# Kernel optimization log

Measured on AMD Instinct MI355X. Metric: run time of the kernel, lower is better.

## Reference

```python
import jax, jax.numpy as jnp
import numpy as np

# Module config (mirrors TritonMoEConfig)
N_EMBD = 768
EXPERT_SIZES = [(8, 512), (8, 1024)]  # (count, width) pairs
TOP_K = 8
NORM_TOPK_PROB = True

EXPERT_WIDTHS = []
for cnt, w in EXPERT_SIZES:
    EXPERT_WIDTHS += [w] * cnt
EXPERT_OFFSETS = np.concatenate([[0], np.cumsum(EXPERT_WIDTHS)]).astype(np.int64)
NUM_EXPERTS = len(EXPERT_WIDTHS)          # 16
TOTAL_WIDTH = int(EXPERT_OFFSETS[-1])     # 12288


def setup_inputs() -> dict:
    key = jax.random.key(0)
    k1, k2, k3, k4 = jax.random.split(key, 4)
    x = jax.random.normal(k1, (1, 2048, N_EMBD), dtype=jnp.float32)
    # trunc_normal(std=0.02) approximated by clipped normal
    router_w = jax.random.normal(k2, (NUM_EXPERTS, N_EMBD), dtype=jnp.float32) * 0.02
    w1 = jnp.clip(jax.random.normal(k3, (N_EMBD, TOTAL_WIDTH), dtype=jnp.float32) * 0.02, -0.06, 0.06)
    w2 = jnp.clip(jax.random.normal(k4, (TOTAL_WIDTH, N_EMBD), dtype=jnp.float32) * 0.02, -0.06, 0.06)
    return {"x": x, "router_w": router_w, "w1": w1, "w2": w2}


def reference(x, router_w, w1, w2):
    B, S, D = x.shape
    xt = x.reshape(-1, D)                              # [T, D]
    T = xt.shape[0]
    # 1. Route tokens: softmax over experts, top-k selection
    logits = jnp.einsum('td,ed->te', xt, router_w)     # [T, E]
    probs = jax.nn.softmax(logits, axis=-1)
    topk_w, topk_idx = jax.lax.top_k(probs, TOP_K)     # [T, K]
    if NORM_TOPK_PROB:
        topk_w = topk_w / jnp.sum(topk_w, axis=-1, keepdims=True)
    # Per-token combine weight for every expert (0 if not selected): [T, E]
    comb = jnp.zeros((T, NUM_EXPERTS), dtype=xt.dtype)
    comb = comb.at[jnp.arange(T)[:, None], topk_idx].add(topk_w)
    # 2-6. Grouped GEMM up (with activation) + down, combine with routing weights.
    # Experts have distinct widths, so loop over the fixed expert list.
    out = jnp.zeros_like(xt)
    for e in range(NUM_EXPERTS):
        off = int(EXPERT_OFFSETS[e])
        wd = EXPERT_WIDTHS[e]
        h = jax.nn.gelu(xt @ w1[:, off:off + wd])      # [T, wd]
        out = out + comb[:, e:e + 1] * (h @ w2[off:off + wd, :])
    return out.reshape(B, S, D)
```

## Files before the change

### kernel.cpp

```cpp
#include <hip/hip_runtime.h>
#include <hip/hip_bf16.h>


#define T_TOK 2048
#define D_EMB 768
#define W_TOT 12288
#define N_EXP 16

typedef __attribute__((ext_vector_type(4))) float f32x4;
typedef __attribute__((ext_vector_type(8))) short bf16x8;

typedef __attribute__((address_space(1))) const unsigned int as1c_u32;
typedef __attribute__((address_space(3))) unsigned int as3_u32;

__device__ __forceinline__ void gload16(const void* g, void* l) {
  __builtin_amdgcn_global_load_lds((as1c_u32*)g, (as3_u32*)l, 16, 0, 0);
}

__device__ __forceinline__ unsigned short f2bf(float f) {
  __hip_bfloat16 h = __float2bfloat16(f);
  return *reinterpret_cast<unsigned short*>(&h);
}

__device__ __forceinline__ float gelu_f(float x) {
  float x3 = x * x * x;
  float a = 0.7978845608028654f * __builtin_fmaf(0.044715f, x3, x);
  a = fminf(fmaxf(a, -20.f), 20.f);
  float e = __expf(-2.0f * a);
  float t = (1.0f - e) / (1.0f + e);
  return 0.5f * x * (1.0f + t);
}

__global__ __launch_bounds__(256) void transpose_cvt_kernel(
    const float* __restrict__ in, unsigned short* __restrict__ out, int R, int C) {
  __shared__ float tile[32][33];
  int c0 = blockIdx.x * 32;
  int r0 = blockIdx.y * 32;
  int i = threadIdx.x;
  {
    int r = i >> 3, c4 = (i & 7) * 4;
    float4 v = *(const float4*)(in + (size_t)(r0 + r) * C + c0 + c4);
    tile[r][c4 + 0] = v.x; tile[r][c4 + 1] = v.y;
    tile[r][c4 + 2] = v.z; tile[r][c4 + 3] = v.w;
  }
  __syncthreads();
  {
    int c = i >> 3, r4 = (i & 7) * 4;
    ushort4 o;
    o.x = f2bf(tile[r4 + 0][c]);
    o.y = f2bf(tile[r4 + 1][c]);
    o.z = f2bf(tile[r4 + 2][c]);
    o.w = f2bf(tile[r4 + 3][c]);
    *(ushort4*)(out + (size_t)(c0 + c) * R + r0 + r4) = o;
  }
}


__global__ __launch_bounds__(256) void router_kernel(
    const float* __restrict__ x, const float* __restrict__ rw,
    float* __restrict__ comb, unsigned short* __restrict__ xbout) {
  int tid = threadIdx.x, lane = tid & 63, w = tid >> 6;
  int t = blockIdx.x * 4 + w;
  const float* xr = x + (size_t)t * D_EMB;
  float xv[12];
#pragma unroll
  for (int i = 0; i < 12; ++i) xv[i] = xr[lane + 64 * i];
#pragma unroll
  for (int i = 0; i < 12; ++i)
    xbout[(size_t)t * D_EMB + lane + 64 * i] = f2bf(xv[i]);
  float lg[16];
#pragma unroll
  for (int e = 0; e < 16; ++e) {
    const float* we = rw + (size_t)e * D_EMB;
    float p = 0.f;
#pragma unroll
    for (int i = 0; i < 12; ++i) p = __builtin_fmaf(xv[i], we[lane + 64 * i], p);
#pragma unroll
    for (int off = 32; off >= 1; off >>= 1) p += __shfl_xor(p, off, 64);
    lg[e] = p;
  }
  float mx = lg[0];
#pragma unroll
  for (int e = 1; e < 16; ++e) mx = fmaxf(mx, lg[e]);
  float ex[16];
#pragma unroll
  for (int e = 0; e < 16; ++e) ex[e] = __expf(lg[e] - mx);
  float selsum = 0.f, myval = 0.f;
#pragma unroll
  for (int e = 0; e < 16; ++e) {
    int rank = 0;
#pragma unroll
    for (int e2 = 0; e2 < 16; ++e2)
      rank += (ex[e2] > ex[e]) || (ex[e2] == ex[e] && e2 < e);
    bool sel = rank < 8;
    float v = sel ? ex[e] : 0.f;
    selsum += v;
    if (e == lane) myval = v;
  }
  if (lane < 16) comb[(size_t)t * N_EXP + lane] = myval / selsum;
}


template <int EPI, int MAP>
__global__ __launch_bounds__(512, 2) void gemm_kernel(
    const unsigned short* __restrict__ Ag, const unsigned short* __restrict__ Bg,
    int lda, int ldb, int ntiles, int kchunk,
    const float* __restrict__ comb, unsigned short* __restrict__ hout,
    float* __restrict__ pout) {
  __shared__ __align__(16) char smem[114688];

  const int tid = threadIdx.x;
  const int lane = tid & 63;
  const int wid = tid >> 6;
  const int wr = wid >> 2;
  const int wc = wid & 3;

  int mt, nt, zt;
  {
    int bid = blockIdx.x;
    if (MAP == 0) {
      int xcd = bid & 7, r = bid >> 3;
      nt = xcd * 8 + (r >> 3); mt = r & 7; zt = 0;
    } else {
      zt = bid & 7; int r = bid >> 3;
      nt = r & 3; mt = r >> 2;
    }
  }
  const int rm0 = mt * 256;
  const int cn0 = nt * 192;
  const int kbeg = zt * kchunk;

  auto gsrc = [&](const unsigned short* base, int ld, int row0, int j) {
    int off = j * 8192 + tid * 16;
    int row = off >> 7, inrow = off & 127;
    int scol = inrow ^ ((row & 7) << 4);
    return (const char*)base + ((size_t)(row0 + row) * ld + kbeg) * 2 + scol;
  };
  const char* pA0 = gsrc(Ag, lda, rm0, 0);
  const char* pA1 = gsrc(Ag, lda, rm0, 1);
  const char* pA2 = gsrc(Ag, lda, rm0, 2);
  const char* pA3 = gsrc(Ag, lda, rm0, 3);
  const char* pB0 = gsrc(Bg, ldb, cn0, 0);
  const char* pB1 = gsrc(Bg, ldb, cn0, 1);
  const char* pB2 = gsrc(Bg, ldb, cn0, 2);

  const int lswz = (lane & 7) << 4;
  const int colk0 = (((lane >> 4) & 3) * 16) ^ lswz;
  const int colk1 = (64 + ((lane >> 4) & 3) * 16) ^ lswz;
  const int abase0 = wr * 16384 + (lane & 15) * 128 + colk0;
  const int abase1 = wr * 16384 + (lane & 15) * 128 + colk1;
  const int bb0 = wc * 6144 + (lane & 15) * 128 + colk0;
  const int bb1 = wc * 6144 + (lane & 15) * 128 + colk1;

  f32x4 acc[8][3];
#pragma unroll
  for (int m = 0; m < 8; ++m)
#pragma unroll
    for (int n = 0; n < 3; ++n) acc[m][n] = (f32x4){0.f, 0.f, 0.f, 0.f};

  gload16(pB0, smem + 65536 + wid * 1024);
  gload16(pB1, smem + 65536 + 8192 + wid * 1024);
  gload16(pB2, smem + 65536 + 16384 + wid * 1024);
  gload16(pA0, smem + wid * 1024);
  gload16(pA2, smem + 16384 + wid * 1024);
  gload16(pA1, smem + 8192 + wid * 1024);
  gload16(pA3, smem + 24576 + wid * 1024);
  pA0 += 128; pA1 += 128; pA2 += 128; pA3 += 128;
  pB0 += 128; pB1 += 128; pB2 += 128;
  __builtin_amdgcn_sched_barrier(0);

  int aoff = 0, boff = 0;
  bf16x8 af[4], ag[4], bfr[3], bgr[3];
  for (int t = 0; t < ntiles; ++t) {
    const int adst = aoff ^ 32768;
    const int bdst = boff ^ 24576;

    asm volatile("s_waitcnt vmcnt(2)" ::: "memory");
    __builtin_amdgcn_s_barrier();
    __builtin_amdgcn_sched_barrier(0);
#pragma unroll
    for (int m = 0; m < 4; ++m) {
      af[m] = *(const bf16x8*)(smem + aoff + abase0 + m * 2048);
      ag[m] = *(const bf16x8*)(smem + aoff + abase1 + m * 2048);
    }
#pragma unroll
    for (int n = 0; n < 3; ++n) {
      bfr[n] = *(const bf16x8*)(smem + 65536 + boff + bb0 + n * 2048);
      bgr[n] = *(const bf16x8*)(smem + 65536 + boff + bb1 + n * 2048);
    }
    gload16(pB0, smem + 65536 + bdst + wid * 1024);
    gload16(pB1, smem + 65536 + bdst + 8192 + wid * 1024);
    gload16(pB2, smem + 65536 + bdst + 16384 + wid * 1024);
    gload16(pA0, smem + adst + wid * 1024);
    gload16(pA2, smem + adst + 16384 + wid * 1024);
    __builtin_amdgcn_sched_barrier(0);
    __builtin_amdgcn_s_setprio(1);
#pragma unroll
    for (int m = 0; m < 4; ++m)
#pragma unroll
      for (int n = 0; n < 3; ++n) {
        acc[m][n] = __builtin_amdgcn_mfma_f32_16x16x32_bf16(af[m], bfr[n], acc[m][n], 0, 0, 0);
        acc[m][n] = __builtin_amdgcn_mfma_f32_16x16x32_bf16(ag[m], bgr[n], acc[m][n], 0, 0, 0);
      }
    __builtin_amdgcn_s_setprio(0);

    asm volatile("s_waitcnt vmcnt(5)" ::: "memory");
    __builtin_amdgcn_s_barrier();
    __builtin_amdgcn_sched_barrier(0);
#pragma unroll
    for (int m = 0; m < 4; ++m) {
      af[m] = *(const bf16x8*)(smem + aoff + abase0 + 8192 + m * 2048);
      ag[m] = *(const bf16x8*)(smem + aoff + abase1 + 8192 + m * 2048);
    }
    gload16(pA1, smem + adst + 8192 + wid * 1024);
    gload16(pA3, smem + adst + 24576 + wid * 1024);
    __builtin_amdgcn_sched_barrier(0);
    __builtin_amdgcn_s_setprio(1);
#pragma unroll
    for (int m = 0; m < 4; ++m)
#pragma unroll
      for (int n = 0; n < 3; ++n) {
        acc[4 + m][n] = __builtin_amdgcn_mfma_f32_16x16x32_bf16(af[m], bfr[n], acc[4 + m][n], 0, 0, 0);
        acc[4 + m][n] = __builtin_amdgcn_mfma_f32_16x16x32_bf16(ag[m], bgr[n], acc[4 + m][n], 0, 0, 0);
      }
    __builtin_amdgcn_s_setprio(0);

    pA0 += 128; pA1 += 128; pA2 += 128; pA3 += 128;
    pB0 += 128; pB1 += 128; pB2 += 128;
    aoff = adst; boff = bdst;
  }

  asm volatile("s_waitcnt vmcnt(0)" ::: "memory");
  __syncthreads();

  const int r0 = (lane >> 4) * 4;
  const int cl = lane & 15;
  if constexpr (EPI == 1) {
    float* Cwf = (float*)smem;
    {
      int row = tid >> 1, c8 = (tid & 1) * 8;
      const float* s = comb + (size_t)(rm0 + row) * N_EXP + c8;
      *(float4*)&Cwf[row * 16 + c8] = *(const float4*)s;
      *(float4*)&Cwf[row * 16 + c8 + 4] = *(const float4*)(s + 4);
    }
    __syncthreads();
#pragma unroll
    for (int n = 0; n < 3; ++n) {
      int colg = cn0 + wc * 48 + n * 16 + cl;
      int e = (colg < 4096) ? (colg >> 9) : (8 + ((colg - 4096) >> 10));
#pragma unroll
      for (int m = 0; m < 8; ++m) {
        int rl = wr * 128 + m * 16 + r0;
#pragma unroll
        for (int r = 0; r < 4; ++r) {
          float v = gelu_f(acc[m][n][r]) * Cwf[(rl + r) * 16 + e];
          hout[(size_t)(rm0 + rl + r) * W_TOT + colg] = f2bf(v);
        }
      }
    }
  } else {
    float* pz = pout + (size_t)zt * T_TOK * D_EMB;
#pragma unroll
    for (int n = 0; n < 3; ++n) {
      int colg = cn0 + wc * 48 + n * 16 + cl;
#pragma unroll
      for (int m = 0; m < 8; ++m) {
        int rl = wr * 128 + m * 16 + r0;
#pragma unroll
        for (int r = 0; r < 4; ++r)
          pz[(size_t)(rm0 + rl + r) * D_EMB + colg] = acc[m][n][r];
      }
    }
  }
}

__global__ __launch_bounds__(256) void reduce_kernel(
    const float* __restrict__ partial, float* __restrict__ out, int splits) {
  int i = (blockIdx.x * 256 + threadIdx.x) * 4;
  if (i >= T_TOK * D_EMB) return;
  float4 s = *(const float4*)(partial + i);
  for (int sp = 1; sp < splits; ++sp) {
    float4 v = *(const float4*)(partial + (size_t)sp * T_TOK * D_EMB + i);
    s.x += v.x; s.y += v.y; s.z += v.z; s.w += v.w;
  }
  *(float4*)(out + i) = s;
}


extern "C" void kernel_launch(void* const* d_in, const int* in_sizes, int n_in,
                              void* d_out, int out_size, void* d_ws, size_t ws_size,
                              hipStream_t stream) {
  const float* x = (const float*)d_in[0];
  const float* router_w = (const float*)d_in[1];
  const float* w1 = (const float*)d_in[2];
  const float* w2 = (const float*)d_in[3];
  float* out = (float*)d_out;

  char* ws = (char*)d_ws;
  size_t off = 0;
  auto alloc = [&](size_t bytes) {
    char* p = ws + off;
    off += (bytes + 255) & ~(size_t)255;
    return p;
  };
  unsigned short* xb  = (unsigned short*)alloc((size_t)T_TOK * D_EMB * 2);
  unsigned short* w1t = (unsigned short*)alloc((size_t)W_TOT * D_EMB * 2);
  unsigned short* w2t = (unsigned short*)alloc((size_t)D_EMB * W_TOT * 2);
  unsigned short* h   = (unsigned short*)alloc((size_t)T_TOK * W_TOT * 2);
  float* comb         = (float*)alloc((size_t)T_TOK * N_EXP * 4);

  const int splits = 8;
  float* partial = (float*)alloc((size_t)splits * T_TOK * D_EMB * 4);
  int kchunk = W_TOT / splits;

  transpose_cvt_kernel<<<dim3(W_TOT / 32, D_EMB / 32), 256, 0, stream>>>(w1, w1t, D_EMB, W_TOT);
  transpose_cvt_kernel<<<dim3(D_EMB / 32, W_TOT / 32), 256, 0, stream>>>(w2, w2t, W_TOT, D_EMB);
  router_kernel<<<T_TOK / 4, 256, 0, stream>>>(x, router_w, comb, xb);

  gemm_kernel<1, 0><<<512, 512, 0, stream>>>(
      xb, w1t, D_EMB, D_EMB, D_EMB / 64, D_EMB, comb, h, nullptr);

  gemm_kernel<0, 1><<<256, 512, 0, stream>>>(
      h, w2t, W_TOT, W_TOT, kchunk / 64, kchunk, nullptr, nullptr, partial);

  reduce_kernel<<<(T_TOK * D_EMB) / 1024, 256, 0, stream>>>(partial, out, splits);
}
```

Before: 136.9 us.

## Enlarge GEMM tile to 256x256 with four-phase quadrant-staged LDS pipeline

Widens the GEMM output tile from 256x192 to 256x256, so each wave holds an 8x4 accumulator block and the grids shrink to 384 and 192 blocks. The main loop is restructured into four sub-phases that each compute one quadrant of the accumulators while staging the next A and B halves into LDS. LDS grows to 128 KB and sync points are re-placed with extra barriers and lgkmcnt waits. The goal is higher arithmetic intensity and fewer blocks. The costs are more barriers, less occupancy (the 128 KB LDS likely allows one block per CU despite launch_bounds 2), and a grid smaller than two waves.

```diff
diff --git a/kernel.cpp b/kernel.cpp
--- a/kernel.cpp
+++ b/kernel.cpp
@@ -107,7 +107,7 @@
     int lda, int ldb, int ntiles, int kchunk,
     const float* __restrict__ comb, unsigned short* __restrict__ hout,
     float* __restrict__ pout) {
-  __shared__ __align__(16) char smem[114688];
+  __shared__ __align__(16) char smem[131072];
 
   const int tid = threadIdx.x;
   const int lane = tid & 63;
@@ -120,114 +120,171 @@
     int bid = blockIdx.x;
     if (MAP == 0) {
       int xcd = bid & 7, r = bid >> 3;
-      nt = xcd * 8 + (r >> 3); mt = r & 7; zt = 0;
+      nt = xcd * 6 + (r >> 3); mt = r & 7; zt = 0;
     } else {
       zt = bid & 7; int r = bid >> 3;
-      nt = r & 3; mt = r >> 2;
+      nt = r % 3; mt = r / 3;
     }
   }
   const int rm0 = mt * 256;
-  const int cn0 = nt * 192;
+  const int cn0 = nt * 256;
   const int kbeg = zt * kchunk;
 
-  auto gsrc = [&](const unsigned short* base, int ld, int row0, int j) {
+  auto gsrcA = [&](int h, int j) {
     int off = j * 8192 + tid * 16;
     int row = off >> 7, inrow = off & 127;
     int scol = inrow ^ ((row & 7) << 4);
-    return (const char*)base + ((size_t)(row0 + row) * ld + kbeg) * 2 + scol;
+    return (const char*)Ag +
+           ((size_t)(rm0 + h * 128 + row) * lda + kbeg) * 2 + scol;
   };
-  const char* pA0 = gsrc(Ag, lda, rm0, 0);
-  const char* pA1 = gsrc(Ag, lda, rm0, 1);
-  const char* pA2 = gsrc(Ag, lda, rm0, 2);
-  const char* pA3 = gsrc(Ag, lda, rm0, 3);
-  const char* pB0 = gsrc(Bg, ldb, cn0, 0);
-  const char* pB1 = gsrc(Bg, ldb, cn0, 1);
-  const char* pB2 = gsrc(Bg, ldb, cn0, 2);
+  auto gsrcB = [&](int h, int j) {
+    int off = j * 8192 + tid * 16;
+    int row = off >> 7, inrow = off & 127;
+    int scol = inrow ^ ((row & 7) << 4);
+    return (const char*)Bg +
+           ((size_t)(cn0 + h * 128 + row) * ldb + kbeg) * 2 + scol;
+  };
+  const char* qA00 = gsrcA(0, 0); const char* qA01 = gsrcA(0, 1);
+  const char* qA10 = gsrcA(1, 0); const char* qA11 = gsrcA(1, 1);
+  const char* qB00 = gsrcB(0, 0); const char* qB01 = gsrcB(0, 1);
+  const char* qB10 = gsrcB(1, 0); const char* qB11 = gsrcB(1, 1);
 
   const int lswz = (lane & 7) << 4;
   const int colk0 = (((lane >> 4) & 3) * 16) ^ lswz;
   const int colk1 = (64 + ((lane >> 4) & 3) * 16) ^ lswz;
-  const int abase0 = wr * 16384 + (lane & 15) * 128 + colk0;
-  const int abase1 = wr * 16384 + (lane & 15) * 128 + colk1;
-  const int bb0 = wc * 6144 + (lane & 15) * 128 + colk0;
-  const int bb1 = wc * 6144 + (lane & 15) * 128 + colk1;
-
-  f32x4 acc[8][3];
+  const int ab0 = wr * 16384 + (lane & 15) * 128 + colk0;
+  const int ab1 = wr * 16384 + (lane & 15) * 128 + colk1;
+  const int bb0 = 65536 + (wc >> 1) * 16384 + ((wc & 1) * 64 + (lane & 15)) * 128 + colk0;
+  const int bb1 = 65536 + (wc >> 1) * 16384 + ((wc & 1) * 64 + (lane & 15)) * 128 + colk1;
+
+  f32x4 acc[8][4];
 #pragma unroll
   for (int m = 0; m < 8; ++m)
 #pragma unroll
-    for (int n = 0; n < 3; ++n) acc[m][n] = (f32x4){0.f, 0.f, 0.f, 0.f};
-
-  gload16(pB0, smem + 65536 + wid * 1024);
-  gload16(pB1, smem + 65536 + 8192 + wid * 1024);
-  gload16(pB2, smem + 65536 + 16384 + wid * 1024);
-  gload16(pA0, smem + wid * 1024);
-  gload16(pA2, smem + 16384 + wid * 1024);
-  gload16(pA1, smem + 8192 + wid * 1024);
-  gload16(pA3, smem + 24576 + wid * 1024);
-  pA0 += 128; pA1 += 128; pA2 += 128; pA3 += 128;
-  pB0 += 128; pB1 += 128; pB2 += 128;
+    for (int n = 0; n < 4; ++n) acc[m][n] = (f32x4){0.f, 0.f, 0.f, 0.f};
+
+  gload16(qA00, smem + 0 + wid * 1024);
+  gload16(qA01, smem + 8192 + wid * 1024);
+  gload16(qA10, smem + 16384 + wid * 1024);
+  gload16(qA11, smem + 16384 + 8192 + wid * 1024);
+  gload16(qB00, smem + 65536 + wid * 1024);
+  gload16(qB01, smem + 65536 + 8192 + wid * 1024);
+  gload16(qB10, smem + 65536 + 16384 + wid * 1024);
+  gload16(qB11, smem + 65536 + 16384 + 8192 + wid * 1024);
+  gload16(qB00 + 128, smem + 65536 + 32768 + wid * 1024);
+  gload16(qB01 + 128, smem + 65536 + 32768 + 8192 + wid * 1024);
+  gload16(qB10 + 128, smem + 65536 + 32768 + 16384 + wid * 1024);
+  gload16(qB11 + 128, smem + 65536 + 32768 + 16384 + 8192 + wid * 1024);
+  const char* pA00 = qA00 + 128; const char* pA01 = qA01 + 128;
+  const char* pA10 = qA10 + 128; const char* pA11 = qA11 + 128;
+  const char* pB00 = qB00 + 256; const char* pB01 = qB01 + 256;
+  const char* pB10 = qB10 + 256; const char* pB11 = qB11 + 256;
+  asm volatile("s_waitcnt vmcnt(4)" ::: "memory");
+  __builtin_amdgcn_s_barrier();
   __builtin_amdgcn_sched_barrier(0);
 
-  int aoff = 0, boff = 0;
-  bf16x8 af[4], ag[4], bfr[3], bgr[3];
+  bf16x8 a[4][2], b0[2][2], b1[2][2];
+  int cb = 0;
   for (int t = 0; t < ntiles; ++t) {
-    const int adst = aoff ^ 32768;
-    const int bdst = boff ^ 24576;
-
-    asm volatile("s_waitcnt vmcnt(2)" ::: "memory");
-    __builtin_amdgcn_s_barrier();
-    __builtin_amdgcn_sched_barrier(0);
+    const int nb = cb ^ 32768;
+
 #pragma unroll
     for (int m = 0; m < 4; ++m) {
-      af[m] = *(const bf16x8*)(smem + aoff + abase0 + m * 2048);
-      ag[m] = *(const bf16x8*)(smem + aoff + abase1 + m * 2048);
-    }
-#pragma unroll
-    for (int n = 0; n < 3; ++n) {
-      bfr[n] = *(const bf16x8*)(smem + 65536 + boff + bb0 + n * 2048);
-      bgr[n] = *(const bf16x8*)(smem + 65536 + boff + bb1 + n * 2048);
-    }
-    gload16(pB0, smem + 65536 + bdst + wid * 1024);
-    gload16(pB1, smem + 65536 + bdst + 8192 + wid * 1024);
-    gload16(pB2, smem + 65536 + bdst + 16384 + wid * 1024);
-    gload16(pA0, smem + adst + wid * 1024);
-    gload16(pA2, smem + adst + 16384 + wid * 1024);
+      a[m][0] = *(const bf16x8*)(smem + cb + ab0 + m * 2048);
+      a[m][1] = *(const bf16x8*)(smem + cb + ab1 + m * 2048);
+    }
+#pragma unroll
+    for (int n = 0; n < 2; ++n) {
+      b0[n][0] = *(const bf16x8*)(smem + cb + bb0 + n * 2048);
+      b0[n][1] = *(const bf16x8*)(smem + cb + bb1 + n * 2048);
+    }
+    gload16(pA00, smem + nb + wid * 1024);
+    gload16(pA01, smem + nb + 8192 + wid * 1024);
+    pA00 += 128; pA01 += 128;
+    __builtin_amdgcn_s_barrier();
+    asm volatile("s_waitcnt lgkmcnt(0)" ::: "memory");
     __builtin_amdgcn_sched_barrier(0);
     __builtin_amdgcn_s_setprio(1);
 #pragma unroll
     for (int m = 0; m < 4; ++m)
 #pragma unroll
-      for (int n = 0; n < 3; ++n) {
-        acc[m][n] = __builtin_amdgcn_mfma_f32_16x16x32_bf16(af[m], bfr[n], acc[m][n], 0, 0, 0);
-        acc[m][n] = __builtin_amdgcn_mfma_f32_16x16x32_bf16(ag[m], bgr[n], acc[m][n], 0, 0, 0);
-      }
+      for (int n = 0; n < 2; ++n)
+#pragma unroll
+        for (int kk = 0; kk < 2; ++kk)
+          acc[m][n] = __builtin_amdgcn_mfma_f32_16x16x32_bf16(
+              a[m][kk], b0[n][kk], acc[m][n], 0, 0, 0);
     __builtin_amdgcn_s_setprio(0);
-
-    asm volatile("s_waitcnt vmcnt(5)" ::: "memory");
-    __builtin_amdgcn_s_barrier();
-    __builtin_amdgcn_sched_barrier(0);
+    __builtin_amdgcn_s_barrier();
+    __builtin_amdgcn_sched_barrier(0);
+
+#pragma unroll
+    for (int n = 0; n < 2; ++n) {
+      b1[n][0] = *(const bf16x8*)(smem + cb + bb0 + 4096 + n * 2048);
+      b1[n][1] = *(const bf16x8*)(smem + cb + bb1 + 4096 + n * 2048);
+    }
+    gload16(pA10, smem + nb + 16384 + wid * 1024);
+    gload16(pA11, smem + nb + 16384 + 8192 + wid * 1024);
+    pA10 += 128; pA11 += 128;
+    __builtin_amdgcn_s_barrier();
+    asm volatile("s_waitcnt lgkmcnt(0)" ::: "memory");
+    __builtin_amdgcn_sched_barrier(0);
+    __builtin_amdgcn_s_setprio(1);
+#pragma unroll
+    for (int m = 0; m < 4; ++m)
+#pragma unroll
+      for (int n = 0; n < 2; ++n)
+#pragma unroll
+        for (int kk = 0; kk < 2; ++kk)
+          acc[m][2 + n] = __builtin_amdgcn_mfma_f32_16x16x32_bf16(
+              a[m][kk], b1[n][kk], acc[m][2 + n], 0, 0, 0);
+    __builtin_amdgcn_s_setprio(0);
+    __builtin_amdgcn_s_barrier();
+    __builtin_amdgcn_sched_barrier(0);
+
 #pragma unroll
     for (int m = 0; m < 4; ++m) {
-      af[m] = *(const bf16x8*)(smem + aoff + abase0 + 8192 + m * 2048);
-      ag[m] = *(const bf16x8*)(smem + aoff + abase1 + 8192 + m * 2048);
-    }
-    gload16(pA1, smem + adst + 8192 + wid * 1024);
-    gload16(pA3, smem + adst + 24576 + wid * 1024);
+      a[m][0] = *(const bf16x8*)(smem + cb + ab0 + 8192 + m * 2048);
+      a[m][1] = *(const bf16x8*)(smem + cb + ab1 + 8192 + m * 2048);
+    }
+    gload16(pB00, smem + 65536 + cb + wid * 1024);
+    gload16(pB01, smem + 65536 + cb + 8192 + wid * 1024);
+    pB00 += 128; pB01 += 128;
+    __builtin_amdgcn_s_barrier();
+    asm volatile("s_waitcnt lgkmcnt(0)" ::: "memory");
     __builtin_amdgcn_sched_barrier(0);
     __builtin_amdgcn_s_setprio(1);
 #pragma unroll
     for (int m = 0; m < 4; ++m)
 #pragma unroll
-      for (int n = 0; n < 3; ++n) {
-        acc[4 + m][n] = __builtin_amdgcn_mfma_f32_16x16x32_bf16(af[m], bfr[n], acc[4 + m][n], 0, 0, 0);
-        acc[4 + m][n] = __builtin_amdgcn_mfma_f32_16x16x32_bf16(ag[m], bgr[n], acc[4 + m][n], 0, 0, 0);
-      }
+      for (int n = 0; n < 2; ++n)
+#pragma unroll
+        for (int kk = 0; kk < 2; ++kk)
+          acc[4 + m][2 + n] = __builtin_amdgcn_mfma_f32_16x16x32_bf16(
+              a[m][kk], b1[n][kk], acc[4 + m][2 + n], 0, 0, 0);
     __builtin_amdgcn_s_setprio(0);
-
-    pA0 += 128; pA1 += 128; pA2 += 128; pA3 += 128;
-    pB0 += 128; pB1 += 128; pB2 += 128;
-    aoff = adst; boff = bdst;
+    __builtin_amdgcn_s_barrier();
+    __builtin_amdgcn_sched_barrier(0);
+
+    gload16(pB10, smem + 65536 + cb + 16384 + wid * 1024);
+    gload16(pB11, smem + 65536 + cb + 16384 + 8192 + wid * 1024);
+    pB10 += 128; pB11 += 128;
+    asm volatile("s_waitcnt vmcnt(4)" ::: "memory");
+    __builtin_amdgcn_s_barrier();
+    __builtin_amdgcn_sched_barrier(0);
+    __builtin_amdgcn_s_setprio(1);
+#pragma unroll
+    for (int m = 0; m < 4; ++m)
+#pragma unroll
+      for (int n = 0; n < 2; ++n)
+#pragma unroll
+        for (int kk = 0; kk < 2; ++kk)
+          acc[4 + m][n] = __builtin_amdgcn_mfma_f32_16x16x32_bf16(
+              a[m][kk], b0[n][kk], acc[4 + m][n], 0, 0, 0);
+    __builtin_amdgcn_s_setprio(0);
+    __builtin_amdgcn_s_barrier();
+    __builtin_amdgcn_sched_barrier(0);
+
+    cb = nb;
   }
 
   asm volatile("s_waitcnt vmcnt(0)" ::: "memory");
@@ -245,8 +302,8 @@
     }
     __syncthreads();
 #pragma unroll
-    for (int n = 0; n < 3; ++n) {
-      int colg = cn0 + wc * 48 + n * 16 + cl;
+    for (int n = 0; n < 4; ++n) {
+      int colg = cn0 + wc * 64 + n * 16 + cl;
       int e = (colg < 4096) ? (colg >> 9) : (8 + ((colg - 4096) >> 10));
 #pragma unroll
       for (int m = 0; m < 8; ++m) {
@@ -261,8 +318,8 @@
   } else {
     float* pz = pout + (size_t)zt * T_TOK * D_EMB;
 #pragma unroll
-    for (int n = 0; n < 3; ++n) {
-      int colg = cn0 + wc * 48 + n * 16 + cl;
+    for (int n = 0; n < 4; ++n) {
+      int colg = cn0 + wc * 64 + n * 16 + cl;
 #pragma unroll
       for (int m = 0; m < 8; ++m) {
         int rl = wr * 128 + m * 16 + r0;
@@ -317,10 +374,10 @@
   transpose_cvt_kernel<<<dim3(D_EMB / 32, W_TOT / 32), 256, 0, stream>>>(w2, w2t, W_TOT, D_EMB);
   router_kernel<<<T_TOK / 4, 256, 0, stream>>>(x, router_w, comb, xb);
 
-  gemm_kernel<1, 0><<<512, 512, 0, stream>>>(
+  gemm_kernel<1, 0><<<384, 512, 0, stream>>>(
       xb, w1t, D_EMB, D_EMB, D_EMB / 64, D_EMB, comb, h, nullptr);
 
-  gemm_kernel<0, 1><<<256, 512, 0, stream>>>(
+  gemm_kernel<0, 1><<<192, 512, 0, stream>>>(
       h, w2t, W_TOT, W_TOT, kchunk / 64, kchunk, nullptr, nullptr, partial);
 
   reduce_kernel<<<(T_TOK * D_EMB) / 1024, 256, 0, stream>>>(partial, out, splits);
```

Result: slower. 158.9 us (+16.0%).

## Shrink GEMM tiles to 256x128 with K=32 steps for higher occupancy

Applied to the files above, without the earlier changes.

Reworks both grouped GEMMs to use 256x128 output tiles with a 32-wide K step, so the kernel needs 48 KB of LDS instead of 112 KB and launch bounds allow 4 blocks per CU. It also changes the swizzle and load mapping, makes the leading dimension a template constant, and raises the down-projection split-K from 8 to 16 when workspace allows. The aim is more resident waves and more blocks to hide latency and fill the CUs. The trade-off is less data reuse per tile, twice the barriers per K, and a larger partial buffer for the reduce kernel to sum.

```diff
diff --git a/kernel.cpp b/kernel.cpp
--- a/kernel.cpp
+++ b/kernel.cpp
@@ -101,13 +101,13 @@
 }
 
 
-template <int EPI, int MAP>
-__global__ __launch_bounds__(512, 2) void gemm_kernel(
+template <int EPI, int MAP, int LD>
+__global__ __launch_bounds__(512, 4) void gemm_kernel(
     const unsigned short* __restrict__ Ag, const unsigned short* __restrict__ Bg,
-    int lda, int ldb, int ntiles, int kchunk,
+    int ntiles, int kchunk, int splits,
     const float* __restrict__ comb, unsigned short* __restrict__ hout,
     float* __restrict__ pout) {
-  __shared__ __align__(16) char smem[114688];
+  __shared__ __align__(16) char smem[49152];
 
   const int tid = threadIdx.x;
   const int lane = tid & 63;
@@ -120,114 +120,82 @@
     int bid = blockIdx.x;
     if (MAP == 0) {
       int xcd = bid & 7, r = bid >> 3;
-      nt = xcd * 8 + (r >> 3); mt = r & 7; zt = 0;
+      nt = xcd * 12 + (r >> 3); mt = r & 7; zt = 0;
     } else {
-      zt = bid & 7; int r = bid >> 3;
-      nt = r & 3; mt = r >> 2;
+      zt = bid % splits; int rr = bid / splits;
+      nt = rr % 6; mt = rr / 6;
     }
   }
   const int rm0 = mt * 256;
-  const int cn0 = nt * 192;
+  const int cn0 = nt * 128;
   const int kbeg = zt * kchunk;
 
-  auto gsrc = [&](const unsigned short* base, int ld, int row0, int j) {
-    int off = j * 8192 + tid * 16;
-    int row = off >> 7, inrow = off & 127;
-    int scol = inrow ^ ((row & 7) << 4);
-    return (const char*)base + ((size_t)(row0 + row) * ld + kbeg) * 2 + scol;
-  };
-  const char* pA0 = gsrc(Ag, lda, rm0, 0);
-  const char* pA1 = gsrc(Ag, lda, rm0, 1);
-  const char* pA2 = gsrc(Ag, lda, rm0, 2);
-  const char* pA3 = gsrc(Ag, lda, rm0, 3);
-  const char* pB0 = gsrc(Bg, ldb, cn0, 0);
-  const char* pB1 = gsrc(Bg, ldb, cn0, 1);
-  const char* pB2 = gsrc(Bg, ldb, cn0, 2);
-
-  const int lswz = (lane & 7) << 4;
-  const int colk0 = (((lane >> 4) & 3) * 16) ^ lswz;
-  const int colk1 = (64 + ((lane >> 4) & 3) * 16) ^ lswz;
-  const int abase0 = wr * 16384 + (lane & 15) * 128 + colk0;
-  const int abase1 = wr * 16384 + (lane & 15) * 128 + colk1;
-  const int bb0 = wc * 6144 + (lane & 15) * 128 + colk0;
-  const int bb1 = wc * 6144 + (lane & 15) * 128 + colk1;
-
-  f32x4 acc[8][3];
+  const int s = tid >> 2;
+  const int scol = ((tid & 3) ^ (s & 3)) << 4;
+  const int rA = (s & 63) + ((s >> 6) << 7);
+  const char* pA0 = (const char*)Ag + ((size_t)(rm0 + rA) * LD + kbeg) * 2 + scol;
+  const char* pA1 = pA0 + (size_t)64 * LD * 2;
+  const char* pB  = (const char*)Bg + ((size_t)(cn0 + s) * LD + kbeg) * 2 + scol;
+
+  const int slot = ((lane >> 4) ^ (lane & 3)) << 4;
+  const int abase = wr * 4096 + (lane & 15) * 64 + slot;
+  const int bbase = 32768 + (wc * 32 + (lane & 15)) * 64 + slot;
+
+  f32x4 acc[8][2];
 #pragma unroll
   for (int m = 0; m < 8; ++m)
 #pragma unroll
-    for (int n = 0; n < 3; ++n) acc[m][n] = (f32x4){0.f, 0.f, 0.f, 0.f};
-
-  gload16(pB0, smem + 65536 + wid * 1024);
-  gload16(pB1, smem + 65536 + 8192 + wid * 1024);
-  gload16(pB2, smem + 65536 + 16384 + wid * 1024);
+    for (int n = 0; n < 2; ++n) acc[m][n] = (f32x4){0.f, 0.f, 0.f, 0.f};
+
+  gload16(pB, smem + 32768 + wid * 1024);
   gload16(pA0, smem + wid * 1024);
-  gload16(pA2, smem + 16384 + wid * 1024);
   gload16(pA1, smem + 8192 + wid * 1024);
-  gload16(pA3, smem + 24576 + wid * 1024);
-  pA0 += 128; pA1 += 128; pA2 += 128; pA3 += 128;
-  pB0 += 128; pB1 += 128; pB2 += 128;
+  pB += 64; pA0 += 64; pA1 += 64;
   __builtin_amdgcn_sched_barrier(0);
 
   int aoff = 0, boff = 0;
-  bf16x8 af[4], ag[4], bfr[3], bgr[3];
+  bf16x8 a[4], b[2];
   for (int t = 0; t < ntiles; ++t) {
-    const int adst = aoff ^ 32768;
-    const int bdst = boff ^ 24576;
+    const int nA = aoff ^ 16384;
+    const int nB = boff ^ 8192;
+
+    asm volatile("s_waitcnt vmcnt(1)" ::: "memory");
+    __builtin_amdgcn_s_barrier();
+    __builtin_amdgcn_sched_barrier(0);
+#pragma unroll
+    for (int m = 0; m < 4; ++m)
+      a[m] = *(const bf16x8*)(smem + aoff + abase + m * 1024);
+    b[0] = *(const bf16x8*)(smem + boff + bbase);
+    b[1] = *(const bf16x8*)(smem + boff + bbase + 1024);
+    gload16(pB, smem + 32768 + nB + wid * 1024);
+    gload16(pA0, smem + nA + wid * 1024);
+    __builtin_amdgcn_sched_barrier(0);
+    __builtin_amdgcn_s_setprio(1);
+#pragma unroll
+    for (int m = 0; m < 4; ++m) {
+      acc[m][0] = __builtin_amdgcn_mfma_f32_16x16x32_bf16(a[m], b[0], acc[m][0], 0, 0, 0);
+      acc[m][1] = __builtin_amdgcn_mfma_f32_16x16x32_bf16(a[m], b[1], acc[m][1], 0, 0, 0);
+    }
+    __builtin_amdgcn_s_setprio(0);
 
     asm volatile("s_waitcnt vmcnt(2)" ::: "memory");
     __builtin_amdgcn_s_barrier();
     __builtin_amdgcn_sched_barrier(0);
 #pragma unroll
+    for (int m = 0; m < 4; ++m)
+      a[m] = *(const bf16x8*)(smem + aoff + 8192 + abase + m * 1024);
+    gload16(pA1, smem + nA + 8192 + wid * 1024);
+    pB += 64; pA0 += 64; pA1 += 64;
+    __builtin_amdgcn_sched_barrier(0);
+    __builtin_amdgcn_s_setprio(1);
+#pragma unroll
     for (int m = 0; m < 4; ++m) {
-      af[m] = *(const bf16x8*)(smem + aoff + abase0 + m * 2048);
-      ag[m] = *(const bf16x8*)(smem + aoff + abase1 + m * 2048);
-    }
-#pragma unroll
-    for (int n = 0; n < 3; ++n) {
-      bfr[n] = *(const bf16x8*)(smem + 65536 + boff + bb0 + n * 2048);
-      bgr[n] = *(const bf16x8*)(smem + 65536 + boff + bb1 + n * 2048);
-    }
-    gload16(pB0, smem + 65536 + bdst + wid * 1024);
-    gload16(pB1, smem + 65536 + bdst + 8192 + wid * 1024);
-    gload16(pB2, smem + 65536 + bdst + 16384 + wid * 1024);
-    gload16(pA0, smem + adst + wid * 1024);
-    gload16(pA2, smem + adst + 16384 + wid * 1024);
-    __builtin_amdgcn_sched_barrier(0);
-    __builtin_amdgcn_s_setprio(1);
-#pragma unroll
-    for (int m = 0; m < 4; ++m)
-#pragma unroll
-      for (int n = 0; n < 3; ++n) {
-        acc[m][n] = __builtin_amdgcn_mfma_f32_16x16x32_bf16(af[m], bfr[n], acc[m][n], 0, 0, 0);
-        acc[m][n] = __builtin_amdgcn_mfma_f32_16x16x32_bf16(ag[m], bgr[n], acc[m][n], 0, 0, 0);
-      }
+      acc[4 + m][0] = __builtin_amdgcn_mfma_f32_16x16x32_bf16(a[m], b[0], acc[4 + m][0], 0, 0, 0);
+      acc[4 + m][1] = __builtin_amdgcn_mfma_f32_16x16x32_bf16(a[m], b[1], acc[4 + m][1], 0, 0, 0);
+    }
     __builtin_amdgcn_s_setprio(0);
 
-    asm volatile("s_waitcnt vmcnt(5)" ::: "memory");
-    __builtin_amdgcn_s_barrier();
-    __builtin_amdgcn_sched_barrier(0);
-#pragma unroll
-    for (int m = 0; m < 4; ++m) {
-      af[m] = *(const bf16x8*)(smem + aoff + abase0 + 8192 + m * 2048);
-      ag[m] = *(const bf16x8*)(smem + aoff + abase1 + 8192 + m * 2048);
-    }
-    gload16(pA1, smem + adst + 8192 + wid * 1024);
-    gload16(pA3, smem + adst + 24576 + wid * 1024);
-    __builtin_amdgcn_sched_barrier(0);
-    __builtin_amdgcn_s_setprio(1);
-#pragma unroll
-    for (int m = 0; m < 4; ++m)
-#pragma unroll
-      for (int n = 0; n < 3; ++n) {
-        acc[4 + m][n] = __builtin_amdgcn_mfma_f32_16x16x32_bf16(af[m], bfr[n], acc[4 + m][n], 0, 0, 0);
-        acc[4 + m][n] = __builtin_amdgcn_mfma_f32_16x16x32_bf16(ag[m], bgr[n], acc[4 + m][n], 0, 0, 0);
-      }
-    __builtin_amdgcn_s_setprio(0);
-
-    pA0 += 128; pA1 += 128; pA2 += 128; pA3 += 128;
-    pB0 += 128; pB1 += 128; pB2 += 128;
-    aoff = adst; boff = bdst;
+    aoff = nA; boff = nB;
   }
 
   asm volatile("s_waitcnt vmcnt(0)" ::: "memory");
@@ -239,14 +207,14 @@
     float* Cwf = (float*)smem;
     {
       int row = tid >> 1, c8 = (tid & 1) * 8;
-      const float* s = comb + (size_t)(rm0 + row) * N_EXP + c8;
-      *(float4*)&Cwf[row * 16 + c8] = *(const float4*)s;
-      *(float4*)&Cwf[row * 16 + c8 + 4] = *(const float4*)(s + 4);
+      const float* sc = comb + (size_t)(rm0 + row) * N_EXP + c8;
+      *(float4*)&Cwf[row * 16 + c8] = *(const float4*)sc;
+      *(float4*)&Cwf[row * 16 + c8 + 4] = *(const float4*)(sc + 4);
     }
     __syncthreads();
 #pragma unroll
-    for (int n = 0; n < 3; ++n) {
-      int colg = cn0 + wc * 48 + n * 16 + cl;
+    for (int n = 0; n < 2; ++n) {
+      int colg = cn0 + wc * 32 + n * 16 + cl;
       int e = (colg < 4096) ? (colg >> 9) : (8 + ((colg - 4096) >> 10));
 #pragma unroll
       for (int m = 0; m < 8; ++m) {
@@ -261,8 +229,8 @@
   } else {
     float* pz = pout + (size_t)zt * T_TOK * D_EMB;
 #pragma unroll
-    for (int n = 0; n < 3; ++n) {
-      int colg = cn0 + wc * 48 + n * 16 + cl;
+    for (int n = 0; n < 2; ++n) {
+      int colg = cn0 + wc * 32 + n * 16 + cl;
 #pragma unroll
       for (int m = 0; m < 8; ++m) {
         int rl = wr * 128 + m * 16 + r0;
@@ -278,12 +246,12 @@
     const float* __restrict__ partial, float* __restrict__ out, int splits) {
   int i = (blockIdx.x * 256 + threadIdx.x) * 4;
   if (i >= T_TOK * D_EMB) return;
-  float4 s = *(const float4*)(partial + i);
+  float4 sv = *(const float4*)(partial + i);
   for (int sp = 1; sp < splits; ++sp) {
     float4 v = *(const float4*)(partial + (size_t)sp * T_TOK * D_EMB + i);
-    s.x += v.x; s.y += v.y; s.z += v.z; s.w += v.w;
-  }
-  *(float4*)(out + i) = s;
+    sv.x += v.x; sv.y += v.y; sv.z += v.z; sv.w += v.w;
+  }
+  *(float4*)(out + i) = sv;
 }
 
 
@@ -309,7 +277,9 @@
   unsigned short* h   = (unsigned short*)alloc((size_t)T_TOK * W_TOT * 2);
   float* comb         = (float*)alloc((size_t)T_TOK * N_EXP * 4);
 
-  const int splits = 8;
+  int splits = 16;
+  if (off + (size_t)16 * T_TOK * D_EMB * 4 > ws_size) splits = 8;
+  if (off + (size_t)8 * T_TOK * D_EMB * 4 > ws_size) splits = 4;
   float* partial = (float*)alloc((size_t)splits * T_TOK * D_EMB * 4);
   int kchunk = W_TOT / splits;
 
@@ -317,11 +287,11 @@
   transpose_cvt_kernel<<<dim3(D_EMB / 32, W_TOT / 32), 256, 0, stream>>>(w2, w2t, W_TOT, D_EMB);
   router_kernel<<<T_TOK / 4, 256, 0, stream>>>(x, router_w, comb, xb);
 
-  gemm_kernel<1, 0><<<512, 512, 0, stream>>>(
-      xb, w1t, D_EMB, D_EMB, D_EMB / 64, D_EMB, comb, h, nullptr);
-
-  gemm_kernel<0, 1><<<256, 512, 0, stream>>>(
-      h, w2t, W_TOT, W_TOT, kchunk / 64, kchunk, nullptr, nullptr, partial);
+  gemm_kernel<1, 0, D_EMB><<<768, 512, 0, stream>>>(
+      xb, w1t, D_EMB / 32, D_EMB, 1, comb, h, nullptr);
+
+  gemm_kernel<0, 1, W_TOT><<<48 * splits, 512, 0, stream>>>(
+      h, w2t, kchunk / 32, kchunk, splits, nullptr, nullptr, partial);
 
   reduce_kernel<<<(T_TOK * D_EMB) / 1024, 256, 0, stream>>>(partial, out, splits);
 }
```

Result: slower. 163.1 us (+19.1%).

## Replace dense GEMMs with token-gathered grouped MoE GEMMs over routed tokens

Applied to the files above, without the earlier changes.

The router now builds per-expert token lists with atomics, storing token, top-k slot and combine weight, in place of a dense combine matrix. Both GEMMs become grouped per-expert GEMMs. The up-projection gathers routed token rows and writes a compact per-expert h buffer, and the down-projection scatters rows into per-slot partial buffers, which an 8-way reduction then sums. Because each token picks 8 of 16 experts, this skips about half of the dense FLOPs. In exchange it adds gather/scatter indirection, padding to 256-row tiles, nondeterministic token ordering from the atomics, and a larger 256x256 tile with 128KB of shared memory.

```diff
diff --git a/kernel.cpp b/kernel.cpp
--- a/kernel.cpp
+++ b/kernel.cpp
@@ -58,7 +58,8 @@
 
 __global__ __launch_bounds__(256) void router_kernel(
     const float* __restrict__ x, const float* __restrict__ rw,
-    float* __restrict__ comb, unsigned short* __restrict__ xbout) {
+    unsigned short* __restrict__ xbout, int* __restrict__ toklist,
+    float* __restrict__ combw, int* __restrict__ cnt) {
   int tid = threadIdx.x, lane = tid & 63, w = tid >> 6;
   int t = blockIdx.x * 4 + w;
   const float* xr = x + (size_t)t * D_EMB;
@@ -86,6 +87,7 @@
 #pragma unroll
   for (int e = 0; e < 16; ++e) ex[e] = __expf(lg[e] - mx);
   float selsum = 0.f, myval = 0.f;
+  bool mysel = false;
 #pragma unroll
   for (int e = 0; e < 16; ++e) {
     int rank = 0;
@@ -95,19 +97,26 @@
     bool sel = rank < 8;
     float v = sel ? ex[e] : 0.f;
     selsum += v;
-    if (e == lane) myval = v;
-  }
-  if (lane < 16) comb[(size_t)t * N_EXP + lane] = myval / selsum;
-}
-
-
-template <int EPI, int MAP>
-__global__ __launch_bounds__(512, 2) void gemm_kernel(
-    const unsigned short* __restrict__ Ag, const unsigned short* __restrict__ Bg,
-    int lda, int ldb, int ntiles, int kchunk,
-    const float* __restrict__ comb, unsigned short* __restrict__ hout,
-    float* __restrict__ pout) {
-  __shared__ __align__(16) char smem[114688];
+    if (e == lane) { myval = v; mysel = sel; }
+  }
+  unsigned long long mask = __ballot(lane < 16 && mysel);
+  if (lane < 16 && mysel) {
+    int slot = __popcll(mask & ((1ull << lane) - 1));
+    int pos = atomicAdd(&cnt[lane], 1);
+    toklist[lane * 2048 + pos] = t | (slot << 16);
+    combw[lane * 2048 + pos] = myval / selsum;
+  }
+}
+
+
+template <int MODE>
+__global__ __launch_bounds__(512, 2) void moe_gemm_kernel(
+    const unsigned short* __restrict__ Abase,
+    const unsigned short* __restrict__ Bbase,
+    const int* __restrict__ toklist, const float* __restrict__ combw,
+    const int* __restrict__ cnt, unsigned short* __restrict__ hbuf,
+    float* __restrict__ partial, float* __restrict__ dump) {
+  __shared__ __align__(16) char smem[131072];
 
   const int tid = threadIdx.x;
   const int lane = tid & 63;
@@ -115,171 +124,193 @@
   const int wr = wid >> 2;
   const int wc = wid & 3;
 
-  int mt, nt, zt;
+  int e, W, offe, mt, nt;
+  int hb;
   {
     int bid = blockIdx.x;
-    if (MAP == 0) {
-      int xcd = bid & 7, r = bid >> 3;
-      nt = xcd * 8 + (r >> 3); mt = r & 7; zt = 0;
+    if (MODE == 0) {
+      if (bid < 128) {
+        e = bid >> 4; int r = bid & 15; mt = r >> 1; nt = r & 1;
+        W = 512; offe = e * 512; hb = e * (2048 * 512);
+      } else {
+        int b = bid - 128; int el = b >> 5; int r = b & 31; mt = r >> 2; nt = r & 3;
+        e = el + 8; W = 1024; offe = 4096 + el * 1024;
+        hb = 8 * (2048 * 512) + el * (2048 * 1024);
+      }
     } else {
-      zt = bid & 7; int r = bid >> 3;
-      nt = r & 3; mt = r >> 2;
-    }
-  }
+      int bb = bid;
+      if (bid < 192) {
+        int el = bb / 24; e = el; W = 512; offe = el * 512; hb = el * (2048 * 512);
+        bb -= el * 24;
+      } else {
+        bb -= 192; int el = bb / 24; e = el + 8; W = 1024;
+        offe = 4096 + el * 1024; hb = 8 * (2048 * 512) + el * (2048 * 1024);
+        bb -= el * 24;
+      }
+      mt = bb / 3; nt = bb - mt * 3;
+    }
+  }
+  const int ce = cnt[e];
+  const int cpad = (ce + 255) & ~255;
   const int rm0 = mt * 256;
-  const int cn0 = nt * 192;
-  const int kbeg = zt * kchunk;
-
-  auto gsrc = [&](const unsigned short* base, int ld, int row0, int j) {
-    int off = j * 8192 + tid * 16;
-    int row = off >> 7, inrow = off & 127;
-    int scol = inrow ^ ((row & 7) << 4);
-    return (const char*)base + ((size_t)(row0 + row) * ld + kbeg) * 2 + scol;
-  };
-  const char* pA0 = gsrc(Ag, lda, rm0, 0);
-  const char* pA1 = gsrc(Ag, lda, rm0, 1);
-  const char* pA2 = gsrc(Ag, lda, rm0, 2);
-  const char* pA3 = gsrc(Ag, lda, rm0, 3);
-  const char* pB0 = gsrc(Bg, ldb, cn0, 0);
-  const char* pB1 = gsrc(Bg, ldb, cn0, 1);
-  const char* pB2 = gsrc(Bg, ldb, cn0, 2);
+  if (rm0 >= cpad) return;
+  const int cn0 = nt * 256;
+  const int ntiles = (MODE == 0) ? (D_EMB / 64) : (W >> 6);
+
+  const int srow = tid >> 3;
+  const int scol = ((tid & 7) * 16) ^ ((srow & 7) << 4);
+  const char* pA[4];
+#pragma unroll
+  for (int j = 0; j < 4; ++j) {
+    int i = rm0 + j * 64 + srow;
+    size_t rowoff;
+    if (MODE == 0) {
+      int tok = (i < ce) ? (toklist[e * 2048 + i] & 0xFFFF) : 0;
+      rowoff = (size_t)tok * D_EMB;
+    } else {
+      rowoff = (size_t)hb + (size_t)i * W;
+    }
+    pA[j] = (const char*)Abase + rowoff * 2 + scol;
+  }
+  const char* pB[4];
+#pragma unroll
+  for (int j = 0; j < 4; ++j) {
+    int r = cn0 + j * 64 + srow;
+    size_t rowoff = (MODE == 0) ? ((size_t)(offe + r) * D_EMB)
+                                : ((size_t)r * W_TOT + offe);
+    pB[j] = (const char*)Bbase + rowoff * 2 + scol;
+  }
 
   const int lswz = (lane & 7) << 4;
   const int colk0 = (((lane >> 4) & 3) * 16) ^ lswz;
   const int colk1 = (64 + ((lane >> 4) & 3) * 16) ^ lswz;
-  const int abase0 = wr * 16384 + (lane & 15) * 128 + colk0;
-  const int abase1 = wr * 16384 + (lane & 15) * 128 + colk1;
-  const int bb0 = wc * 6144 + (lane & 15) * 128 + colk0;
-  const int bb1 = wc * 6144 + (lane & 15) * 128 + colk1;
-
-  f32x4 acc[8][3];
+  const int ab0 = wr * 16384 + (lane & 15) * 128 + colk0;
+  const int ab1 = wr * 16384 + (lane & 15) * 128 + colk1;
+  const int bb0 = wc * 8192 + (lane & 15) * 128 + colk0;
+  const int bb1 = wc * 8192 + (lane & 15) * 128 + colk1;
+
+  f32x4 acc[8][4];
 #pragma unroll
   for (int m = 0; m < 8; ++m)
 #pragma unroll
-    for (int n = 0; n < 3; ++n) acc[m][n] = (f32x4){0.f, 0.f, 0.f, 0.f};
-
-  gload16(pB0, smem + 65536 + wid * 1024);
-  gload16(pB1, smem + 65536 + 8192 + wid * 1024);
-  gload16(pB2, smem + 65536 + 16384 + wid * 1024);
-  gload16(pA0, smem + wid * 1024);
-  gload16(pA2, smem + 16384 + wid * 1024);
-  gload16(pA1, smem + 8192 + wid * 1024);
-  gload16(pA3, smem + 24576 + wid * 1024);
-  pA0 += 128; pA1 += 128; pA2 += 128; pA3 += 128;
-  pB0 += 128; pB1 += 128; pB2 += 128;
+    for (int n = 0; n < 4; ++n) acc[m][n] = (f32x4){0.f, 0.f, 0.f, 0.f};
+
+#pragma unroll
+  for (int j = 0; j < 4; ++j) gload16(pB[j], smem + 65536 + j * 8192 + wid * 1024);
+  gload16(pA[0], smem + wid * 1024);
+  gload16(pA[2], smem + 16384 + wid * 1024);
+  gload16(pA[1], smem + 8192 + wid * 1024);
+  gload16(pA[3], smem + 24576 + wid * 1024);
+#pragma unroll
+  for (int j = 0; j < 4; ++j) { pA[j] += 128; pB[j] += 128; }
   __builtin_amdgcn_sched_barrier(0);
 
-  int aoff = 0, boff = 0;
-  bf16x8 af[4], ag[4], bfr[3], bgr[3];
+  int aoff = 0, boff = 65536;
+  bf16x8 af[4], ag[4], bfr[4], bgr[4];
   for (int t = 0; t < ntiles; ++t) {
     const int adst = aoff ^ 32768;
-    const int bdst = boff ^ 24576;
+    const int bdst = boff ^ 32768;
 
     asm volatile("s_waitcnt vmcnt(2)" ::: "memory");
     __builtin_amdgcn_s_barrier();
     __builtin_amdgcn_sched_barrier(0);
 #pragma unroll
     for (int m = 0; m < 4; ++m) {
-      af[m] = *(const bf16x8*)(smem + aoff + abase0 + m * 2048);
-      ag[m] = *(const bf16x8*)(smem + aoff + abase1 + m * 2048);
-    }
-#pragma unroll
-    for (int n = 0; n < 3; ++n) {
-      bfr[n] = *(const bf16x8*)(smem + 65536 + boff + bb0 + n * 2048);
-      bgr[n] = *(const bf16x8*)(smem + 65536 + boff + bb1 + n * 2048);
-    }
-    gload16(pB0, smem + 65536 + bdst + wid * 1024);
-    gload16(pB1, smem + 65536 + bdst + 8192 + wid * 1024);
-    gload16(pB2, smem + 65536 + bdst + 16384 + wid * 1024);
-    gload16(pA0, smem + adst + wid * 1024);
-    gload16(pA2, smem + adst + 16384 + wid * 1024);
+      af[m] = *(const bf16x8*)(smem + aoff + ab0 + m * 2048);
+      ag[m] = *(const bf16x8*)(smem + aoff + ab1 + m * 2048);
+    }
+#pragma unroll
+    for (int n = 0; n < 4; ++n) {
+      bfr[n] = *(const bf16x8*)(smem + boff + bb0 + n * 2048);
+      bgr[n] = *(const bf16x8*)(smem + boff + bb1 + n * 2048);
+    }
+#pragma unroll
+    for (int j = 0; j < 4; ++j) gload16(pB[j], smem + bdst + j * 8192 + wid * 1024);
+    gload16(pA[0], smem + adst + wid * 1024);
+    gload16(pA[2], smem + adst + 16384 + wid * 1024);
     __builtin_amdgcn_sched_barrier(0);
     __builtin_amdgcn_s_setprio(1);
 #pragma unroll
     for (int m = 0; m < 4; ++m)
 #pragma unroll
-      for (int n = 0; n < 3; ++n) {
+      for (int n = 0; n < 4; ++n) {
         acc[m][n] = __builtin_amdgcn_mfma_f32_16x16x32_bf16(af[m], bfr[n], acc[m][n], 0, 0, 0);
         acc[m][n] = __builtin_amdgcn_mfma_f32_16x16x32_bf16(ag[m], bgr[n], acc[m][n], 0, 0, 0);
       }
     __builtin_amdgcn_s_setprio(0);
 
-    asm volatile("s_waitcnt vmcnt(5)" ::: "memory");
+    asm volatile("s_waitcnt vmcnt(6)" ::: "memory");
     __builtin_amdgcn_s_barrier();
     __builtin_amdgcn_sched_barrier(0);
 #pragma unroll
     for (int m = 0; m < 4; ++m) {
-      af[m] = *(const bf16x8*)(smem + aoff + abase0 + 8192 + m * 2048);
-      ag[m] = *(const bf16x8*)(smem + aoff + abase1 + 8192 + m * 2048);
-    }
-    gload16(pA1, smem + adst + 8192 + wid * 1024);
-    gload16(pA3, smem + adst + 24576 + wid * 1024);
+      af[m] = *(const bf16x8*)(smem + aoff + ab0 + 8192 + m * 2048);
+      ag[m] = *(const bf16x8*)(smem + aoff + ab1 + 8192 + m * 2048);
+    }
+    gload16(pA[1], smem + adst + 8192 + wid * 1024);
+    gload16(pA[3], smem + adst + 24576 + wid * 1024);
     __builtin_amdgcn_sched_barrier(0);
     __builtin_amdgcn_s_setprio(1);
 #pragma unroll
     for (int m = 0; m < 4; ++m)
 #pragma unroll
-      for (int n = 0; n < 3; ++n) {
+      for (int n = 0; n < 4; ++n) {
         acc[4 + m][n] = __builtin_amdgcn_mfma_f32_16x16x32_bf16(af[m], bfr[n], acc[4 + m][n], 0, 0, 0);
         acc[4 + m][n] = __builtin_amdgcn_mfma_f32_16x16x32_bf16(ag[m], bgr[n], acc[4 + m][n], 0, 0, 0);
       }
     __builtin_amdgcn_s_setprio(0);
 
-    pA0 += 128; pA1 += 128; pA2 += 128; pA3 += 128;
-    pB0 += 128; pB1 += 128; pB2 += 128;
+#pragma unroll
+    for (int j = 0; j < 4; ++j) { pA[j] += 128; pB[j] += 128; }
     aoff = adst; boff = bdst;
   }
 
   asm volatile("s_waitcnt vmcnt(0)" ::: "memory");
-  __syncthreads();
 
   const int r0 = (lane >> 4) * 4;
   const int cl = lane & 15;
-  if constexpr (EPI == 1) {
-    float* Cwf = (float*)smem;
-    {
-      int row = tid >> 1, c8 = (tid & 1) * 8;
-      const float* s = comb + (size_t)(rm0 + row) * N_EXP + c8;
-      *(float4*)&Cwf[row * 16 + c8] = *(const float4*)s;
-      *(float4*)&Cwf[row * 16 + c8 + 4] = *(const float4*)(s + 4);
-    }
-    __syncthreads();
-#pragma unroll
-    for (int n = 0; n < 3; ++n) {
-      int colg = cn0 + wc * 48 + n * 16 + cl;
-      int e = (colg < 4096) ? (colg >> 9) : (8 + ((colg - 4096) >> 10));
-#pragma unroll
-      for (int m = 0; m < 8; ++m) {
-        int rl = wr * 128 + m * 16 + r0;
-#pragma unroll
-        for (int r = 0; r < 4; ++r) {
-          float v = gelu_f(acc[m][n][r]) * Cwf[(rl + r) * 16 + e];
-          hout[(size_t)(rm0 + rl + r) * W_TOT + colg] = f2bf(v);
-        }
+  if constexpr (MODE == 0) {
+#pragma unroll
+    for (int m = 0; m < 8; ++m) {
+#pragma unroll
+      for (int r = 0; r < 4; ++r) {
+        int i = rm0 + wr * 128 + m * 16 + r0 + r;
+        float wgt = (i < ce) ? combw[e * 2048 + i] : 0.f;
+        unsigned short* hrow = hbuf + (size_t)hb + (size_t)i * W + cn0;
+#pragma unroll
+        for (int n = 0; n < 4; ++n)
+          hrow[wc * 64 + n * 16 + cl] = f2bf(gelu_f(acc[m][n][r]) * wgt);
       }
     }
   } else {
-    float* pz = pout + (size_t)zt * T_TOK * D_EMB;
-#pragma unroll
-    for (int n = 0; n < 3; ++n) {
-      int colg = cn0 + wc * 48 + n * 16 + cl;
-#pragma unroll
-      for (int m = 0; m < 8; ++m) {
-        int rl = wr * 128 + m * 16 + r0;
-#pragma unroll
-        for (int r = 0; r < 4; ++r)
-          pz[(size_t)(rm0 + rl + r) * D_EMB + colg] = acc[m][n][r];
+#pragma unroll
+    for (int m = 0; m < 8; ++m) {
+#pragma unroll
+      for (int r = 0; r < 4; ++r) {
+        int i = rm0 + wr * 128 + m * 16 + r0 + r;
+        int entry = toklist[e * 2048 + i];
+        bool valid = (i < ce);
+        int tok = entry & 0xFFFF;
+        int slot = (entry >> 16) & 7;
+        float* dst = valid
+            ? partial + ((size_t)slot * 2048 + tok) * D_EMB + cn0
+            : dump + cn0 - cn0;
+        if (!valid) dst = dump;
+#pragma unroll
+        for (int n = 0; n < 4; ++n)
+          dst[wc * 64 + n * 16 + cl] = acc[m][n][r];
       }
     }
   }
 }
 
 __global__ __launch_bounds__(256) void reduce_kernel(
-    const float* __restrict__ partial, float* __restrict__ out, int splits) {
+    const float* __restrict__ partial, float* __restrict__ out) {
   int i = (blockIdx.x * 256 + threadIdx.x) * 4;
   if (i >= T_TOK * D_EMB) return;
   float4 s = *(const float4*)(partial + i);
-  for (int sp = 1; sp < splits; ++sp) {
+#pragma unroll
+  for (int sp = 1; sp < 8; ++sp) {
     float4 v = *(const float4*)(partial + (size_t)sp * T_TOK * D_EMB + i);
     s.x += v.x; s.y += v.y; s.z += v.z; s.w += v.w;
   }
@@ -306,22 +337,23 @@
   unsigned short* xb  = (unsigned short*)alloc((size_t)T_TOK * D_EMB * 2);
   unsigned short* w1t = (unsigned short*)alloc((size_t)W_TOT * D_EMB * 2);
   unsigned short* w2t = (unsigned short*)alloc((size_t)D_EMB * W_TOT * 2);
-  unsigned short* h   = (unsigned short*)alloc((size_t)T_TOK * W_TOT * 2);
-  float* comb         = (float*)alloc((size_t)T_TOK * N_EXP * 4);
-
-  const int splits = 8;
-  float* partial = (float*)alloc((size_t)splits * T_TOK * D_EMB * 4);
-  int kchunk = W_TOT / splits;
-
+  unsigned short* hbuf = (unsigned short*)alloc((size_t)T_TOK * W_TOT * 2);
+  int*   toklist = (int*)alloc((size_t)N_EXP * 2048 * 4);
+  float* combw   = (float*)alloc((size_t)N_EXP * 2048 * 4);
+  int*   cnt     = (int*)alloc(64);
+  float* dump    = (float*)alloc(768 * 4);
+  float* partial = (float*)alloc((size_t)8 * T_TOK * D_EMB * 4);
+
+  hipMemsetAsync(cnt, 0, 64, stream);
   transpose_cvt_kernel<<<dim3(W_TOT / 32, D_EMB / 32), 256, 0, stream>>>(w1, w1t, D_EMB, W_TOT);
   transpose_cvt_kernel<<<dim3(D_EMB / 32, W_TOT / 32), 256, 0, stream>>>(w2, w2t, W_TOT, D_EMB);
-  router_kernel<<<T_TOK / 4, 256, 0, stream>>>(x, router_w, comb, xb);
-
-  gemm_kernel<1, 0><<<512, 512, 0, stream>>>(
-      xb, w1t, D_EMB, D_EMB, D_EMB / 64, D_EMB, comb, h, nullptr);
-
-  gemm_kernel<0, 1><<<256, 512, 0, stream>>>(
-      h, w2t, W_TOT, W_TOT, kchunk / 64, kchunk, nullptr, nullptr, partial);
-
-  reduce_kernel<<<(T_TOK * D_EMB) / 1024, 256, 0, stream>>>(partial, out, splits);
-}
+  router_kernel<<<T_TOK / 4, 256, 0, stream>>>(x, router_w, xb, toklist, combw, cnt);
+
+  moe_gemm_kernel<0><<<384, 512, 0, stream>>>(
+      xb, w1t, toklist, combw, cnt, hbuf, nullptr, nullptr);
+
+  moe_gemm_kernel<1><<<384, 512, 0, stream>>>(
+      hbuf, w2t, toklist, nullptr, cnt, nullptr, partial, dump);
+
+  reduce_kernel<<<(T_TOK * D_EMB) / 1024, 256, 0, stream>>>(partial, out);
+}
```

Result: slower. 194.5 us (+42.1%).
